# Kernel tuning notes

Hardware: AMD Instinct MI355X
Metric: run time of the kernel (lower is better)

## Reference

```python
import jax, jax.numpy as jnp
import numpy as np

B, T, D = 2048, 200, 256

def setup_inputs() -> dict:
    key = jax.random.key(0)
    k1, k2, k3, k4, k5 = jax.random.split(key, 5)
    query = jax.random.normal(k1, (B, 1, D), dtype=jnp.float32)
    user_behavior = jax.random.normal(k2, (B, T, D), dtype=jnp.float32)
    mask = jax.random.bernoulli(k3, 0.5, (B, T))
    # nn.Linear weights: linear1 (2D -> D), linear2 (D -> 1), no bias
    W1 = jax.random.normal(k4, (D, 2 * D), dtype=jnp.float32) * (1.0 / np.sqrt(2 * D))
    W2 = jax.random.normal(k5, (1, D), dtype=jnp.float32) * (1.0 / np.sqrt(D))
    return {"query": query, "user_behavior": user_behavior, "mask": mask, "W1": W1, "W2": W2}

def reference(query, user_behavior, mask, W1, W2):
    T_ = user_behavior.shape[1]
    queries = jnp.broadcast_to(query, (query.shape[0], T_, query.shape[2]))  # [B,T,D]
    attn_in = jnp.concatenate([queries, user_behavior], axis=-1)  # [B,T,2D]
    h = jnp.tanh(jnp.einsum('btk,dk->btd', attn_in, W1))          # [B,T,D]
    score = jnp.einsum('btd,od->bot', h, W2)                       # [B,1,T] (transpose(1,2) of [B,T,1])
    # masked_fill with 0 BEFORE softmax, as in the original module
    score = jnp.where(mask[:, None, :], jnp.zeros((), score.dtype), score)
    attn = jax.nn.softmax(score, axis=-1)                          # [B,1,T]
    out = jnp.matmul(attn, user_behavior)                          # [B,1,D]
    return jnp.squeeze(out)                                        # [B,D]
```

## Files before the change

### kernel.cpp

```cpp
#include <hip/hip_runtime.h>
#include <hip/hip_bf16.h>

typedef __bf16 bf16_t;
typedef __bf16 bf16x4_t __attribute__((ext_vector_type(4)));
typedef __bf16 bf16x8  __attribute__((ext_vector_type(8)));
typedef float  f32x4   __attribute__((ext_vector_type(4)));

#define T_LEN 200
#define D_DIM 256

__device__ __forceinline__ float fast_tanh(float x) {
    float e = __expf(2.0f * x);
    return 1.0f - 2.0f / (e + 1.0f);
}

__global__ __launch_bounds__(256) void qpart_kernel(
    const float* __restrict__ Q, const float* __restrict__ W1,
    float* __restrict__ Out)
{
    __shared__ float qs[8][256];
    const int tid = threadIdx.x;
    const int b0  = blockIdx.x * 8;
    for (int idx = tid; idx < 8 * 256; idx += 256)
        qs[idx >> 8][idx & 255] = Q[(size_t)(b0 + (idx >> 8)) * 256 + (idx & 255)];
    __syncthreads();
    float acc[8];
    #pragma unroll
    for (int i = 0; i < 8; ++i) acc[i] = 0.f;
    const f32x4* Wv = (const f32x4*)(W1 + (size_t)tid * 512);
    #pragma unroll 4
    for (int k4 = 0; k4 < 64; ++k4) {
        f32x4 w = Wv[k4];
        #pragma unroll
        for (int bb = 0; bb < 8; ++bb) {
            f32x4 qv = *(const f32x4*)&qs[bb][k4 * 4];
            acc[bb] += qv[0]*w[0] + qv[1]*w[1] + qv[2]*w[2] + qv[3]*w[3];
        }
    }
    #pragma unroll
    for (int bb = 0; bb < 8; ++bb)
        Out[(size_t)(b0 + bb) * 256 + tid] = acc[bb];
}

__global__ __launch_bounds__(256) void convw_kernel(
    const float* __restrict__ W1, bf16_t* __restrict__ bfW)
{
    const int d = blockIdx.x;
    const int k = threadIdx.x;
    bfW[(size_t)d * 256 + k] = (bf16_t)W1[(size_t)d * 512 + 256 + k];
}

template<bool SPLIT>
__global__ __launch_bounds__(512, SPLIT ? 4 : 2) void attn_fused_kernel(
    const float* __restrict__ U,
    const int*   __restrict__ Mask,
    const float* __restrict__ W1,
    const float* __restrict__ W2,
    const bf16_t* __restrict__ bfW,
    float* Out,
    float* __restrict__ WsNum,
    float* __restrict__ WsL)
{
    constexpr int MAXT = SPLIT ? 7 : 13;
    __shared__ bf16_t tiles[MAXT * 16 * 256];
    __shared__ float score_lds[MAXT * 16];
    __shared__ float p_lds[MAXT * 16];
    __shared__ float out_lds[4][256];
    __shared__ float l_lds;

    const int tid  = threadIdx.x;
    const int lane = tid & 63;
    const int wv   = tid >> 6;
    const int lr   = lane & 15;
    const int lg   = lane >> 4;

    int b, t0, ntile;
    if (SPLIT) {
        b = blockIdx.x >> 1;
        const int h = blockIdx.x & 1;
        t0 = h ? 112 : 0;
        ntile = h ? 6 : 7;
    } else {
        b = blockIdx.x; t0 = 0; ntile = 13;
    }
    const int rows = ntile * 16;
    char* const tbase = (char*)tiles;

    if (tid < rows) score_lds[tid] = 0.f;
    if (tid == 0)   l_lds = 0.f;

    {
        const float* Ub = U + (size_t)b * (T_LEN * D_DIM);
        #pragma unroll 2
        for (int r = wv; r < rows; r += 8) {
            const int t = t0 + r;
            bf16x4_t v;
            v[0] = (bf16_t)0.f; v[1] = (bf16_t)0.f;
            v[2] = (bf16_t)0.f; v[3] = (bf16_t)0.f;
            if (t < T_LEN) {
                f32x4 g = *(const f32x4*)(Ub + (size_t)t * 256 + lane * 4);
                v[0] = (bf16_t)g[0]; v[1] = (bf16_t)g[1];
                v[2] = (bf16_t)g[2]; v[3] = (bf16_t)g[3];
            }
            *(bf16x4_t*)(tbase + r * 512 + ((lane * 8) ^ ((r & 7) << 4))) = v;
        }
    }

    bf16x8 bq[2][8];
    float  w2v[2];
    #pragma unroll
    for (int n = 0; n < 2; ++n) {
        const int d = wv * 32 + n * 16 + lr;
        if (SPLIT) {
            #pragma unroll
            for (int kk = 0; kk < 8; ++kk)
                bq[n][kk] = *(const bf16x8*)(bfW + (size_t)d * 256 + kk * 32 + lg * 8);
        } else {
            const float* wrow = W1 + (size_t)d * 512 + 256;
            #pragma unroll
            for (int kk = 0; kk < 8; ++kk) {
                const float* s = wrow + kk * 32 + lg * 8;
                f32x4 lo = *(const f32x4*)s;
                f32x4 hi = *(const f32x4*)(s + 4);
                bf16x8 v;
                v[0]=(bf16_t)lo[0]; v[1]=(bf16_t)lo[1]; v[2]=(bf16_t)lo[2]; v[3]=(bf16_t)lo[3];
                v[4]=(bf16_t)hi[0]; v[5]=(bf16_t)hi[1]; v[6]=(bf16_t)hi[2]; v[7]=(bf16_t)hi[3];
                bq[n][kk] = v;
            }
        }
        w2v[n] = W2[d];
    }
    float qp[2];
    #pragma unroll
    for (int n = 0; n < 2; ++n)
        qp[n] = Out[(size_t)b * 256 + wv * 32 + n * 16 + lr];

    __syncthreads();

    for (int mt = 0; mt < ntile; ++mt) {
        f32x4 acc0 = {0.f,0.f,0.f,0.f}, acc1 = {0.f,0.f,0.f,0.f};
        const int rbase = mt * 16 + lr;
        #pragma unroll
        for (int kk = 0; kk < 8; ++kk) {
            const unsigned aoff = (unsigned)rbase * 512
                + (((unsigned)(kk * 64 + lg * 16)) ^ (((unsigned)lr & 7) << 4));
            bf16x8 a = *(const bf16x8*)(tbase + aoff);
            acc0 = __builtin_amdgcn_mfma_f32_16x16x32_bf16(a, bq[0][kk], acc0, 0, 0, 0);
            acc1 = __builtin_amdgcn_mfma_f32_16x16x32_bf16(a, bq[1][kk], acc1, 0, 0, 0);
        }
        float sp[4];
        #pragma unroll
        for (int r = 0; r < 4; ++r) {
            float h0 = fast_tanh(acc0[r] + qp[0]);
            float h1 = fast_tanh(acc1[r] + qp[1]);
            sp[r] = h0 * w2v[0] + h1 * w2v[1];
        }
        #pragma unroll
        for (int r = 0; r < 4; ++r) {
            sp[r] += __shfl_xor(sp[r], 1);
            sp[r] += __shfl_xor(sp[r], 2);
            sp[r] += __shfl_xor(sp[r], 4);
            sp[r] += __shfl_xor(sp[r], 8);
        }
        if (lr == 0) {
            #pragma unroll
            for (int r = 0; r < 4; ++r)
                atomicAdd(&score_lds[mt * 16 + lg * 4 + r], sp[r]);
        }
    }
    __syncthreads();

    {
        float p = 0.f;
        const int t = t0 + tid;
        if (tid < rows && t < T_LEN)
            p = Mask[(size_t)b * T_LEN + t] ? 1.0f : __expf(score_lds[tid]);
        if (tid < rows) p_lds[tid] = p;
        float ps = p;
        ps += __shfl_xor(ps, 1);
        ps += __shfl_xor(ps, 2);
        ps += __shfl_xor(ps, 4);
        ps += __shfl_xor(ps, 8);
        ps += __shfl_xor(ps, 16);
        ps += __shfl_xor(ps, 32);
        if (lane == 0 && ps != 0.f) atomicAdd(&l_lds, ps);
    }
    __syncthreads();

    {
        const int dp = tid & 127;
        const int jg = tid >> 7;
        const int qr = rows >> 2;
        float o0 = 0.f, o1 = 0.f;
        for (int i = 0; i < qr; ++i) {
            const int j = jg * qr + i;
            const float p = p_lds[j];
            const unsigned w = *(const unsigned*)(tbase + j * 512
                             + (((unsigned)(dp * 4)) ^ (((unsigned)j & 7) << 4)));
            o0 += p * __builtin_bit_cast(float, w << 16);
            o1 += p * __builtin_bit_cast(float, w & 0xffff0000u);
        }
        out_lds[jg][dp * 2]     = o0;
        out_lds[jg][dp * 2 + 1] = o1;
    }
    __syncthreads();

    if (tid < 256) {
        const float num = out_lds[0][tid] + out_lds[1][tid]
                        + out_lds[2][tid] + out_lds[3][tid];
        if (SPLIT) WsNum[(size_t)blockIdx.x * 256 + tid] = num;
        else       Out[(size_t)b * 256 + tid] = num / l_lds;
    }
    if (SPLIT && tid == 0) WsL[blockIdx.x] = l_lds;
}

__global__ __launch_bounds__(256) void combine_kernel(
    const float* __restrict__ WsNum, const float* __restrict__ WsL,
    float* __restrict__ Out)
{
    const int b = blockIdx.x, tid = threadIdx.x;
    const float n = WsNum[(size_t)(2 * b) * 256 + tid]
                  + WsNum[(size_t)(2 * b + 1) * 256 + tid];
    const float l = WsL[2 * b] + WsL[2 * b + 1];
    Out[(size_t)b * 256 + tid] = n / l;
}

extern "C" void kernel_launch(void* const* d_in, const int* in_sizes, int n_in,
                              void* d_out, int out_size, void* d_ws, size_t ws_size,
                              hipStream_t stream)
{
    const float* Q  = (const float*)d_in[0];
    const float* U  = (const float*)d_in[1];
    const int*   Mk = (const int*)d_in[2];
    const float* W1 = (const float*)d_in[3];
    const float* W2 = (const float*)d_in[4];
    float* Out = (float*)d_out;
    const int B = in_sizes[0] / D_DIM;

    qpart_kernel<<<dim3(B / 8), dim3(256), 0, stream>>>(Q, W1, Out);

    const size_t nblk = (size_t)B * 2;
    const size_t need = nblk * 256 * 4
                      + nblk * 4
                      + 256 * 256 * 2;
    if (ws_size >= need) {
        float*  wsn = (float*)d_ws;
        float*  wsl = wsn + nblk * 256;
        bf16_t* bfw = (bf16_t*)(wsl + nblk);
        convw_kernel<<<dim3(256), dim3(256), 0, stream>>>(W1, bfw);
        attn_fused_kernel<true><<<dim3((unsigned)nblk), dim3(512), 0, stream>>>(
            U, Mk, W1, W2, bfw, Out, wsn, wsl);
        combine_kernel<<<dim3(B), dim3(256), 0, stream>>>(wsn, wsl, Out);
    } else {
        attn_fused_kernel<false><<<dim3(B), dim3(512), 0, stream>>>(
            U, Mk, W1, W2, nullptr, Out, nullptr, nullptr);
    }
}
```

Before: 223.3 us.

## Split sequence into four chunks per batch and swap MFMA operand roles

Each batch row is now processed by four blocks of up to 64 time steps instead of two, which shrinks per-block LDS and raises occupancy and parallelism. The combine kernel sums four partials. The MFMA now uses W1 as the A operand and U tiles as B, processing two 16-row tiles per iteration so score reduction needs only cross-group shuffles. It also adds s_setprio around the MFMA loop. The costs are more partial-sum traffic and wasted padding rows in the 56-row chunks.

```diff
diff --git a/kernel.cpp b/kernel.cpp
--- a/kernel.cpp
+++ b/kernel.cpp
@@ -51,7 +51,7 @@
 }
 
 template<bool SPLIT>
-__global__ __launch_bounds__(512, SPLIT ? 4 : 2) void attn_fused_kernel(
+__global__ __launch_bounds__(512, 4) void attn_v5_kernel(
     const float* __restrict__ U,
     const int*   __restrict__ Mask,
     const float* __restrict__ W1,
@@ -61,12 +61,12 @@
     float* __restrict__ WsNum,
     float* __restrict__ WsL)
 {
-    constexpr int MAXT = SPLIT ? 7 : 13;
-    __shared__ bf16_t tiles[MAXT * 16 * 256];
-    __shared__ float score_lds[MAXT * 16];
-    __shared__ float p_lds[MAXT * 16];
+    constexpr int MAXROW = SPLIT ? 64 : 224;
+    __shared__ bf16_t tiles[MAXROW * 256];
+    __shared__ float score_lds[MAXROW];
+    __shared__ float p_lds[MAXROW];
     __shared__ float out_lds[4][256];
-    __shared__ float l_lds;
+    __shared__ float l_red;
 
     const int tid  = threadIdx.x;
     const int lane = tid & 63;
@@ -74,47 +74,29 @@
     const int lr   = lane & 15;
     const int lg   = lane >> 4;
 
-    int b, t0, ntile;
+    int b, t0, nrow, nreal;
     if (SPLIT) {
-        b = blockIdx.x >> 1;
-        const int h = blockIdx.x & 1;
-        t0 = h ? 112 : 0;
-        ntile = h ? 6 : 7;
+        b = blockIdx.x >> 2;
+        const int h = blockIdx.x & 3;
+        t0    = h * 56;
+        nreal = (h == 3) ? 32 : 56;
+        nrow  = (h == 3) ? 32 : 64;
     } else {
-        b = blockIdx.x; t0 = 0; ntile = 13;
-    }
-    const int rows = ntile * 16;
+        b = blockIdx.x; t0 = 0; nreal = 200; nrow = 224;
+    }
     char* const tbase = (char*)tiles;
 
-    if (tid < rows) score_lds[tid] = 0.f;
-    if (tid == 0)   l_lds = 0.f;
-
-    {
-        const float* Ub = U + (size_t)b * (T_LEN * D_DIM);
-        #pragma unroll 2
-        for (int r = wv; r < rows; r += 8) {
-            const int t = t0 + r;
-            bf16x4_t v;
-            v[0] = (bf16_t)0.f; v[1] = (bf16_t)0.f;
-            v[2] = (bf16_t)0.f; v[3] = (bf16_t)0.f;
-            if (t < T_LEN) {
-                f32x4 g = *(const f32x4*)(Ub + (size_t)t * 256 + lane * 4);
-                v[0] = (bf16_t)g[0]; v[1] = (bf16_t)g[1];
-                v[2] = (bf16_t)g[2]; v[3] = (bf16_t)g[3];
-            }
-            *(bf16x4_t*)(tbase + r * 512 + ((lane * 8) ^ ((r & 7) << 4))) = v;
-        }
-    }
-
-    bf16x8 bq[2][8];
-    float  w2v[2];
-    #pragma unroll
-    for (int n = 0; n < 2; ++n) {
-        const int d = wv * 32 + n * 16 + lr;
+    if (tid < nrow) score_lds[tid] = 0.f;
+    if (tid == 0)   l_red = 0.f;
+
+    bf16x8 aw[2][8];
+    #pragma unroll
+    for (int sub = 0; sub < 2; ++sub) {
+        const int d = wv * 32 + sub * 16 + lr;
         if (SPLIT) {
             #pragma unroll
             for (int kk = 0; kk < 8; ++kk)
-                bq[n][kk] = *(const bf16x8*)(bfW + (size_t)d * 256 + kk * 32 + lg * 8);
+                aw[sub][kk] = *(const bf16x8*)(bfW + (size_t)d * 256 + kk * 32 + lg * 8);
         } else {
             const float* wrow = W1 + (size_t)d * 512 + 256;
             #pragma unroll
@@ -125,57 +107,77 @@
                 bf16x8 v;
                 v[0]=(bf16_t)lo[0]; v[1]=(bf16_t)lo[1]; v[2]=(bf16_t)lo[2]; v[3]=(bf16_t)lo[3];
                 v[4]=(bf16_t)hi[0]; v[5]=(bf16_t)hi[1]; v[6]=(bf16_t)hi[2]; v[7]=(bf16_t)hi[3];
-                bq[n][kk] = v;
+                aw[sub][kk] = v;
             }
         }
-        w2v[n] = W2[d];
-    }
-    float qp[2];
-    #pragma unroll
-    for (int n = 0; n < 2; ++n)
-        qp[n] = Out[(size_t)b * 256 + wv * 32 + n * 16 + lr];
-
-    __syncthreads();
-
-    for (int mt = 0; mt < ntile; ++mt) {
-        f32x4 acc0 = {0.f,0.f,0.f,0.f}, acc1 = {0.f,0.f,0.f,0.f};
-        const int rbase = mt * 16 + lr;
+    }
+    float w2v[2][4], qpv[2][4];
+    #pragma unroll
+    for (int sub = 0; sub < 2; ++sub)
+        #pragma unroll
+        for (int r = 0; r < 4; ++r) {
+            const int d = wv * 32 + sub * 16 + lg * 4 + r;
+            w2v[sub][r] = W2[d];
+            qpv[sub][r] = Out[(size_t)b * 256 + d];
+        }
+
+    {
+        const float* Ub = U + (size_t)b * (T_LEN * D_DIM);
+        const int ni = nrow >> 3;
+        for (int i = 0; i < ni; ++i) {
+            const int r = wv + i * 8;
+            bf16x4_t v;
+            v[0]=(bf16_t)0.f; v[1]=(bf16_t)0.f; v[2]=(bf16_t)0.f; v[3]=(bf16_t)0.f;
+            if (r < nreal) {
+                f32x4 g = *(const f32x4*)(Ub + (size_t)(t0 + r) * 256 + lane * 4);
+                v[0]=(bf16_t)g[0]; v[1]=(bf16_t)g[1]; v[2]=(bf16_t)g[2]; v[3]=(bf16_t)g[3];
+            }
+            *(bf16x4_t*)(tbase + r * 512 + ((lane * 8) ^ ((r & 7) << 4))) = v;
+        }
+    }
+    __syncthreads();
+
+    const int npair = nrow >> 5;
+    for (int pp = 0; pp < npair; ++pp) {
+        f32x4 a00 = {0,0,0,0}, a01 = {0,0,0,0};
+        f32x4 a10 = {0,0,0,0}, a11 = {0,0,0,0};
+        const int r0 = pp * 32 + lr;
+        const int r1 = r0 + 16;
+        __builtin_amdgcn_s_setprio(1);
         #pragma unroll
         for (int kk = 0; kk < 8; ++kk) {
-            const unsigned aoff = (unsigned)rbase * 512
-                + (((unsigned)(kk * 64 + lg * 16)) ^ (((unsigned)lr & 7) << 4));
-            bf16x8 a = *(const bf16x8*)(tbase + aoff);
-            acc0 = __builtin_amdgcn_mfma_f32_16x16x32_bf16(a, bq[0][kk], acc0, 0, 0, 0);
-            acc1 = __builtin_amdgcn_mfma_f32_16x16x32_bf16(a, bq[1][kk], acc1, 0, 0, 0);
-        }
-        float sp[4];
+            const unsigned kb = (unsigned)(kk * 64 + lg * 16);
+            bf16x8 u0 = *(const bf16x8*)(tbase + r0 * 512 + (kb ^ (((unsigned)r0 & 7) << 4)));
+            bf16x8 u1 = *(const bf16x8*)(tbase + r1 * 512 + (kb ^ (((unsigned)r1 & 7) << 4)));
+            a00 = __builtin_amdgcn_mfma_f32_16x16x32_bf16(aw[0][kk], u0, a00, 0, 0, 0);
+            a01 = __builtin_amdgcn_mfma_f32_16x16x32_bf16(aw[1][kk], u0, a01, 0, 0, 0);
+            a10 = __builtin_amdgcn_mfma_f32_16x16x32_bf16(aw[0][kk], u1, a10, 0, 0, 0);
+            a11 = __builtin_amdgcn_mfma_f32_16x16x32_bf16(aw[1][kk], u1, a11, 0, 0, 0);
+        }
+        __builtin_amdgcn_s_setprio(0);
+
+        float s0 = 0.f, s1 = 0.f;
         #pragma unroll
         for (int r = 0; r < 4; ++r) {
-            float h0 = fast_tanh(acc0[r] + qp[0]);
-            float h1 = fast_tanh(acc1[r] + qp[1]);
-            sp[r] = h0 * w2v[0] + h1 * w2v[1];
-        }
-        #pragma unroll
-        for (int r = 0; r < 4; ++r) {
-            sp[r] += __shfl_xor(sp[r], 1);
-            sp[r] += __shfl_xor(sp[r], 2);
-            sp[r] += __shfl_xor(sp[r], 4);
-            sp[r] += __shfl_xor(sp[r], 8);
-        }
-        if (lr == 0) {
-            #pragma unroll
-            for (int r = 0; r < 4; ++r)
-                atomicAdd(&score_lds[mt * 16 + lg * 4 + r], sp[r]);
+            s0 += w2v[0][r] * fast_tanh(a00[r] + qpv[0][r]);
+            s0 += w2v[1][r] * fast_tanh(a01[r] + qpv[1][r]);
+            s1 += w2v[0][r] * fast_tanh(a10[r] + qpv[0][r]);
+            s1 += w2v[1][r] * fast_tanh(a11[r] + qpv[1][r]);
+        }
+        s0 += __shfl_xor(s0, 16); s0 += __shfl_xor(s0, 32);
+        s1 += __shfl_xor(s1, 16); s1 += __shfl_xor(s1, 32);
+        if (lg == 0) {
+            atomicAdd(&score_lds[pp * 32 + lr], s0);
+            atomicAdd(&score_lds[pp * 32 + 16 + lr], s1);
         }
     }
     __syncthreads();
 
     {
         float p = 0.f;
-        const int t = t0 + tid;
-        if (tid < rows && t < T_LEN)
-            p = Mask[(size_t)b * T_LEN + t] ? 1.0f : __expf(score_lds[tid]);
-        if (tid < rows) p_lds[tid] = p;
+        if (tid < nreal)
+            p = Mask[(size_t)b * T_LEN + t0 + tid] ? 1.0f : __expf(score_lds[tid]);
+        if (tid < nrow) p_lds[tid] = p;
         float ps = p;
         ps += __shfl_xor(ps, 1);
         ps += __shfl_xor(ps, 2);
@@ -183,14 +185,14 @@
         ps += __shfl_xor(ps, 8);
         ps += __shfl_xor(ps, 16);
         ps += __shfl_xor(ps, 32);
-        if (lane == 0 && ps != 0.f) atomicAdd(&l_lds, ps);
+        if (lane == 0 && ps != 0.f) atomicAdd(&l_red, ps);
     }
     __syncthreads();
 
     {
         const int dp = tid & 127;
         const int jg = tid >> 7;
-        const int qr = rows >> 2;
+        const int qr = nrow >> 2;
         float o0 = 0.f, o1 = 0.f;
         for (int i = 0; i < qr; ++i) {
             const int j = jg * qr + i;
@@ -200,8 +202,7 @@
             o0 += p * __builtin_bit_cast(float, w << 16);
             o1 += p * __builtin_bit_cast(float, w & 0xffff0000u);
         }
-        out_lds[jg][dp * 2]     = o0;
-        out_lds[jg][dp * 2 + 1] = o1;
+        *(float2*)&out_lds[jg][dp * 2] = make_float2(o0, o1);
     }
     __syncthreads();
 
@@ -209,9 +210,9 @@
         const float num = out_lds[0][tid] + out_lds[1][tid]
                         + out_lds[2][tid] + out_lds[3][tid];
         if (SPLIT) WsNum[(size_t)blockIdx.x * 256 + tid] = num;
-        else       Out[(size_t)b * 256 + tid] = num / l_lds;
-    }
-    if (SPLIT && tid == 0) WsL[blockIdx.x] = l_lds;
+        else       Out[(size_t)b * 256 + tid] = num / l_red;
+    }
+    if (SPLIT && tid == 0) WsL[blockIdx.x] = l_red;
 }
 
 __global__ __launch_bounds__(256) void combine_kernel(
@@ -219,9 +220,11 @@
     float* __restrict__ Out)
 {
     const int b = blockIdx.x, tid = threadIdx.x;
-    const float n = WsNum[(size_t)(2 * b) * 256 + tid]
-                  + WsNum[(size_t)(2 * b + 1) * 256 + tid];
-    const float l = WsL[2 * b] + WsL[2 * b + 1];
+    float n = 0.f;
+    #pragma unroll
+    for (int h = 0; h < 4; ++h)
+        n += WsNum[(size_t)(4 * b + h) * 256 + tid];
+    const float l = WsL[4*b] + WsL[4*b+1] + WsL[4*b+2] + WsL[4*b+3];
     Out[(size_t)b * 256 + tid] = n / l;
 }
 
@@ -239,20 +242,18 @@
 
     qpart_kernel<<<dim3(B / 8), dim3(256), 0, stream>>>(Q, W1, Out);
 
-    const size_t nblk = (size_t)B * 2;
-    const size_t need = nblk * 256 * 4
-                      + nblk * 4
-                      + 256 * 256 * 2;
+    const size_t nblk = (size_t)B * 4;
+    const size_t need = nblk * 256 * 4 + nblk * 4 + 256 * 256 * 2;
     if (ws_size >= need) {
         float*  wsn = (float*)d_ws;
         float*  wsl = wsn + nblk * 256;
         bf16_t* bfw = (bf16_t*)(wsl + nblk);
         convw_kernel<<<dim3(256), dim3(256), 0, stream>>>(W1, bfw);
-        attn_fused_kernel<true><<<dim3((unsigned)nblk), dim3(512), 0, stream>>>(
+        attn_v5_kernel<true><<<dim3((unsigned)nblk), dim3(512), 0, stream>>>(
             U, Mk, W1, W2, bfw, Out, wsn, wsl);
         combine_kernel<<<dim3(B), dim3(256), 0, stream>>>(wsn, wsl, Out);
     } else {
-        attn_fused_kernel<false><<<dim3(B), dim3(512), 0, stream>>>(
+        attn_v5_kernel<false><<<dim3(B), dim3(512), 0, stream>>>(
             U, Mk, W1, W2, nullptr, Out, nullptr, nullptr);
     }
 }
```

New measurement: 275.2 us, median of 2. 23.3% more time.
